# Kernel optimization log

Hardware: AMD Instinct MI355X
Metric: run time of the kernel (lower is better)

The kernel has to match this reference:

```python
import jax, jax.numpy as jnp
import numpy as np

LAMBDA_MAX = 2.0  # PyG ChebConv default when lambda_max is None and normalization='sym'
K = 3


def setup_inputs() -> dict:
    key = jax.random.key(0)
    ks = jax.random.split(key, 6)
    B, T, NT, Fin, Fout = 512, 24, 10, 256, 256
    N = B * NT
    E = 163840
    X = jax.random.normal(ks[0], (B, T, NT, Fin), dtype=jnp.float32)
    # edges without self loops (ChebConv removes them before building the Laplacian)
    rng = np.random.default_rng(0)
    src = rng.integers(0, N, size=E)
    off = rng.integers(1, N, size=E)
    dst = (src + off) % N
    edge_index = jnp.asarray(np.stack([src, dst]), dtype=jnp.int32)
    edge_weight = jax.random.uniform(ks[1], (E,), dtype=jnp.float32) + 0.1
    g = float(np.sqrt(6.0 / (Fin + Fout)))
    Ws = jax.random.uniform(ks[2], (4, Fin, Fout), minval=-g, maxval=g, dtype=jnp.float32)
    bs = jnp.zeros((4, Fout), jnp.float32)
    gc = float(np.sqrt(6.0 / (2 * Fout)))
    thetas = jax.random.uniform(ks[3], (4, K, Fout, Fout), minval=-gc, maxval=gc, dtype=jnp.float32)
    conv_bs = jnp.zeros((4, Fout), jnp.float32)
    return dict(X=X, edge_weight=edge_weight, Ws=Ws, bs=bs, thetas=thetas,
                conv_bs=conv_bs, edge_index=edge_index)


def _cheb_norm(edge_index, edge_weight, num_nodes):
    # L_hat = 2/lambda_max * (I - D^-1/2 A D^-1/2) - I
    src, dst = edge_index[0], edge_index[1]
    deg = jax.ops.segment_sum(edge_weight, src, num_segments=num_nodes)
    dis = jnp.where(deg > 0, jax.lax.rsqrt(jnp.where(deg > 0, deg, 1.0)), 0.0)
    w = -dis[src] * edge_weight * dis[dst]          # off-diagonal of L (sym)
    w_hat = (2.0 / LAMBDA_MAX) * w                  # scaled off-diagonal of L_hat
    diag = 2.0 / LAMBDA_MAX - 1.0                   # scalar diagonal of L_hat
    return w_hat, diag


def reference(X, edge_weight, Ws, bs, thetas, conv_bs, edge_index):
    B, T, NT, Fin = X.shape
    Fout = Ws.shape[-1]
    N = B * NT
    Xs = X.reshape(N, T, Fin).transpose(1, 0, 2)  # (T, N, Fin), matches torch .view
    src, dst = edge_index[0], edge_index[1]
    w_hat, diag = _cheb_norm(edge_index, edge_weight, N)

    def prop(x):  # L_hat @ x via edge scatter
        return jax.ops.segment_sum(w_hat[:, None] * x[src], dst, num_segments=N) + diag * x

    def cheb(x, theta, b):
        Tx0 = x
        out = Tx0 @ theta[0]
        Tx1 = prop(Tx0)
        out = out + Tx1 @ theta[1]
        for k in range(2, theta.shape[0]):
            Tx2 = 2.0 * prop(Tx1) - Tx0
            out = out + Tx2 @ theta[k]
            Tx0, Tx1 = Tx1, Tx2
        return out + b

    def step(carry, X_t):
        H, C = carry
        I = jax.nn.sigmoid(X_t @ Ws[0] + cheb(H, thetas[0], conv_bs[0]) + bs[0])
        Fg = jax.nn.sigmoid(X_t @ Ws[1] + cheb(H, thetas[1], conv_bs[1]) + bs[1])
        Tc = jnp.tanh(X_t @ Ws[2] + cheb(H, thetas[2], conv_bs[2]) + bs[2])
        C_new = Fg * C + I * Tc
        O = jax.nn.sigmoid(X_t @ Ws[3] + cheb(H, thetas[3], conv_bs[3]) + bs[3])
        H_new = O * jnp.tanh(C_new)
        return (H_new, C_new), None

    H0 = jnp.zeros((N, Fout), X.dtype)
    (H, C), _ = jax.lax.scan(step, (H0, H0), Xs)
    return H, C
```

## Files before the change

kernel.cpp:

```cpp
#include <hip/hip_runtime.h>
#include <cstddef>
#include <cstdint>

#define N_NODES 5120
#define E_EDGES 163840
#define F 256
#define TSTEPS 24
#define ND 1024
#define XROWSTRIDE 6144

typedef unsigned short u16;
typedef unsigned int u32;
typedef __bf16 bf16x8 __attribute__((ext_vector_type(8)));
typedef float f32x4 __attribute__((ext_vector_type(4)));

__device__ __forceinline__ u16 f2bf(float f) {
    u32 u = __float_as_uint(f);
    u = (u + 0x7FFFu + ((u >> 16) & 1u)) >> 16;
    return (u16)u;
}
__device__ __forceinline__ float bf2f(u16 h) {
    return __uint_as_float((u32)h << 16);
}
__device__ __forceinline__ float fsigmoid(float x) {
    return 1.f / (1.f + __expf(-x));
}
__device__ __forceinline__ float ftanh(float x) {
    return 1.f - 2.f / (__expf(2.f * x) + 1.f);
}


__global__ void deg_kernel(const float* __restrict__ ew, const int* __restrict__ src,
                           float* __restrict__ deg) {
    int e = blockIdx.x * 256 + threadIdx.x;
    if (e < E_EDGES) atomicAdd(&deg[src[e]], ew[e]);
}

__global__ void dis_kernel(float* __restrict__ deg) {
    int n = blockIdx.x * 256 + threadIdx.x;
    if (n < N_NODES) {
        float d = deg[n];
        deg[n] = d > 0.f ? rsqrtf(d) : 0.f;
    }
}

__global__ void count_kernel(const int* __restrict__ dst, int* __restrict__ cnt) {
    int e = blockIdx.x * 256 + threadIdx.x;
    if (e < E_EDGES) atomicAdd(&cnt[dst[e]], 1);
}

__global__ void scan_kernel(const int* __restrict__ cnt, int* __restrict__ row_ptr) {
    __shared__ int s[256];
    int tid = threadIdx.x;
    int base = tid * 20;
    int local[20];
    int sum = 0;
    #pragma unroll
    for (int i = 0; i < 20; i++) { local[i] = sum; sum += cnt[base + i]; }
    s[tid] = sum;
    __syncthreads();
    for (int off = 1; off < 256; off <<= 1) {
        int v = (tid >= off) ? s[tid - off] : 0;
        __syncthreads();
        s[tid] += v;
        __syncthreads();
    }
    int offset = (tid == 0) ? 0 : s[tid - 1];
    #pragma unroll
    for (int i = 0; i < 20; i++) row_ptr[base + i] = offset + local[i];
    if (tid == 0) row_ptr[N_NODES] = E_EDGES;
}

__global__ void fill_csr(const int* __restrict__ src, const int* __restrict__ dst,
                         const float* __restrict__ ew, const float* __restrict__ dis,
                         const int* __restrict__ row_ptr, int* __restrict__ cursor,
                         int* __restrict__ csr_src, float* __restrict__ csr_w) {
    int e = blockIdx.x * 256 + threadIdx.x;
    if (e >= E_EDGES) return;
    int s = src[e], d = dst[e];
    int pos = row_ptr[d] + atomicAdd(&cursor[d], 1);
    csr_src[pos] = s;
    csr_w[pos] = -dis[s] * ew[e] * dis[d];
}

__global__ void build_wcatT(const float* __restrict__ Ws, const float* __restrict__ thetas,
                            u16* __restrict__ WT) {
    int idx = blockIdx.x * 256 + threadIdx.x;
    if (idx >= 1024 * 1024) return;
    int c = idx >> 10, k = idx & 1023;
    int g = (c >> 4) & 3;
    int j = (c >> 6) * 16 + (c & 15);
    float v;
    if (k < 256) {
        v = Ws[(g * 256 + k) * 256 + j];
    } else {
        int kc = (k >> 8) - 1;
        int rr = k & 255;
        v = thetas[((g * 3 + kc) * 256 + rr) * 256 + j];
    }
    WT[idx] = f2bf(v);
}

__global__ void build_bsum(const float* __restrict__ bs, const float* __restrict__ cbs,
                           float* __restrict__ bsum) {
    int c = blockIdx.x * 256 + threadIdx.x;
    if (c >= 1024) return;
    int g = (c >> 4) & 3;
    int j = (c >> 6) * 16 + (c & 15);
    bsum[c] = bs[g * 256 + j] + cbs[g * 256 + j];
}


__global__ __launch_bounds__(256) void prop_kernel(
        const u16* __restrict__ xin, const u16* __restrict__ sub, float scale,
        const int* __restrict__ row_ptr, const int* __restrict__ csr_src,
        const float* __restrict__ csr_w, u16* __restrict__ out_bf,
        const float* __restrict__ X, int t, u16* __restrict__ xt_out) {
    __shared__ int s_src[4][64];
    __shared__ float s_w[4][64];
    int wid = threadIdx.x >> 6, l = threadIdx.x & 63;
    int n = blockIdx.x * 4 + wid;
    int start = row_ptr[n], end = row_ptr[n + 1];
    float acc0 = 0.f, acc1 = 0.f, acc2 = 0.f, acc3 = 0.f;
    int fb = l * 4;
    for (int base = start; base < end; base += 64) {
        int chunk = min(64, end - base);
        if (l < chunk) {
            s_src[wid][l] = csr_src[base + l];
            s_w[wid][l] = csr_w[base + l];
        }
        #pragma unroll 4
        for (int i = 0; i < chunk; i++) {
            int s = s_src[wid][i];
            float wt = s_w[wid][i];
            ushort4 hv = *(const ushort4*)(xin + (size_t)s * F + fb);
            acc0 += wt * bf2f(hv.x);
            acc1 += wt * bf2f(hv.y);
            acc2 += wt * bf2f(hv.z);
            acc3 += wt * bf2f(hv.w);
        }
    }
    size_t o = (size_t)n * F + fb;
    float r0 = scale * acc0, r1 = scale * acc1, r2 = scale * acc2, r3 = scale * acc3;
    if (sub) {
        ushort4 sv = *(const ushort4*)(sub + o);
        r0 -= bf2f(sv.x); r1 -= bf2f(sv.y); r2 -= bf2f(sv.z); r3 -= bf2f(sv.w);
    }
    ushort4 ov;
    ov.x = f2bf(r0); ov.y = f2bf(r1); ov.z = f2bf(r2); ov.w = f2bf(r3);
    *(ushort4*)(out_bf + o) = ov;
    if (xt_out) {
        float4 xv = *(const float4*)(X + (size_t)n * XROWSTRIDE + (size_t)t * F + fb);
        ushort4 xo;
        xo.x = f2bf(xv.x); xo.y = f2bf(xv.y); xo.z = f2bf(xv.z); xo.w = f2bf(xv.w);
        *(ushort4*)(xt_out + o) = xo;
    }
}

#define GBM 64
#define GBN 128
#define GBK 64

__global__ __launch_bounds__(256) void mfma_gemm(
        const u16* __restrict__ Xt, const u16* __restrict__ Hb,
        const u16* __restrict__ T1, const u16* __restrict__ T2,
        const u16* __restrict__ WT, const float* __restrict__ bsum,
        float* __restrict__ Cst, float* __restrict__ Hout, u16* __restrict__ HbNew,
        int writeH) {
    __shared__ alignas(16) u16 As[GBM * GBK];
    __shared__ alignas(16) u16 Bs[GBN * GBK];
    int tid = threadIdx.x;
    int w = tid >> 6, l = tid & 63;
    int m0 = blockIdx.x * GBM, n0 = blockIdx.y * GBN;
    int wm = (w >> 1) * 32, wn = (w & 1) * 64;

    int srow = l >> 3;
    int scol = 8 * ((l & 7) ^ srow);

    f32x4 acc[2][4] = {};

    for (int k0 = 0; k0 < 1024; k0 += GBK) {
        int seg = k0 >> 8;
        const u16* ab = (seg == 0) ? Xt : (seg == 1) ? Hb : (seg == 2) ? T1 : T2;
        ab += (k0 & 255);
        const u16* bb = WT + k0;
        #pragma unroll
        for (int i = 0; i < 2; i++) {
            int c = i * 4 + w;
            int row = c * 8 + srow;
            __builtin_amdgcn_global_load_lds(
                (const __attribute__((address_space(1))) u32*)(ab + (size_t)(m0 + row) * F + scol),
                (__attribute__((address_space(3))) u32*)(As + c * 512), 16, 0, 0);
        }
        #pragma unroll
        for (int i = 0; i < 4; i++) {
            int c = i * 4 + w;
            int row = c * 8 + srow;
            __builtin_amdgcn_global_load_lds(
                (const __attribute__((address_space(1))) u32*)(bb + (size_t)(n0 + row) * 1024 + scol),
                (__attribute__((address_space(3))) u32*)(Bs + c * 512), 16, 0, 0);
        }
        __syncthreads();
        #pragma unroll
        for (int kk = 0; kk < 2; kk++) {
            int kr = kk * 32 + (l >> 4) * 8;
            bf16x8 af[2], bfr[4];
            #pragma unroll
            for (int mf = 0; mf < 2; mf++) {
                int r = wm + mf * 16 + (l & 15);
                af[mf] = *(const bf16x8*)(As + r * GBK + (kr ^ ((r & 7) << 3)));
            }
            #pragma unroll
            for (int nf = 0; nf < 4; nf++) {
                int r = wn + nf * 16 + (l & 15);
                bfr[nf] = *(const bf16x8*)(Bs + r * GBK + (kr ^ ((r & 7) << 3)));
            }
            #pragma unroll
            for (int mf = 0; mf < 2; mf++)
                #pragma unroll
                for (int nf = 0; nf < 4; nf++)
                    acc[mf][nf] = __builtin_amdgcn_mfma_f32_16x16x32_bf16(
                        af[mf], bfr[nf], acc[mf][nf], 0, 0, 0);
        }
        __syncthreads();
    }

    int cr = (l >> 4) * 4, cc = l & 15;
    int feat = ((n0 >> 6) + (w & 1)) * 16 + cc;
    float bI = bsum[n0 + wn + 0  + cc];
    float bF = bsum[n0 + wn + 16 + cc];
    float bT = bsum[n0 + wn + 32 + cc];
    float bO = bsum[n0 + wn + 48 + cc];
    #pragma unroll
    for (int mf = 0; mf < 2; mf++) {
        #pragma unroll
        for (int r = 0; r < 4; r++) {
            int row = m0 + wm + mf * 16 + cr + r;
            size_t o = (size_t)row * F + feat;
            float I  = fsigmoid(acc[mf][0][r] + bI);
            float Fg = fsigmoid(acc[mf][1][r] + bF);
            float Tc = ftanh(acc[mf][2][r] + bT);
            float O  = fsigmoid(acc[mf][3][r] + bO);
            float c  = Fg * Cst[o] + I * Tc;
            Cst[o] = c;
            float h = O * ftanh(c);
            if (writeH) Hout[o] = h;
            HbNew[o] = f2bf(h);
        }
    }
}


extern "C" void kernel_launch(void* const* d_in, const int* in_sizes, int n_in,
                              void* d_out, int out_size, void* d_ws, size_t ws_size,
                              hipStream_t stream) {
    const float* X   = (const float*)d_in[0];
    const float* ew  = (const float*)d_in[1];
    const float* Ws  = (const float*)d_in[2];
    const float* bs  = (const float*)d_in[3];
    const float* th  = (const float*)d_in[4];
    const float* cbs = (const float*)d_in[5];
    const int*   ei  = (const int*)d_in[6];
    const int* src = ei;
    const int* dst = ei + E_EDGES;

    float* H = (float*)d_out;
    float* C = H + (size_t)N_NODES * F;

    char* w = (char*)d_ws;
    size_t off = 0;
    auto alloc = [&](size_t bytes) {
        void* p = w + off;
        off += (bytes + 255) & ~(size_t)255;
        return p;
    };
    float* deg     = (float*)alloc(N_NODES * 4);
    int*   cnt     = (int*)  alloc(N_NODES * 4);
    int*   cursor  = (int*)  alloc(N_NODES * 4);
    int*   row_ptr = (int*)  alloc((N_NODES + 1) * 4);
    int*   csr_src = (int*)  alloc(E_EDGES * 4);
    float* csr_w   = (float*)alloc(E_EDGES * 4);
    u16*   WT      = (u16*)  alloc((size_t)1024 * 1024 * 2);
    float* bsum    = (float*)alloc(1024 * 4);
    u16*   Xtbf    = (u16*)  alloc((size_t)N_NODES * F * 2);
    u16*   Hb0     = (u16*)  alloc((size_t)N_NODES * F * 2);
    u16*   Hb1     = (u16*)  alloc((size_t)N_NODES * F * 2);
    u16*   Tx1bf   = (u16*)  alloc((size_t)N_NODES * F * 2);
    u16*   Tx2bf   = (u16*)  alloc((size_t)N_NODES * F * 2);

    hipMemsetAsync(d_out, 0, (size_t)2 * N_NODES * F * 4, stream);
    hipMemsetAsync(Hb0, 0, (size_t)N_NODES * F * 2, stream);
    hipMemsetAsync(deg, 0, N_NODES * 4, stream);
    hipMemsetAsync(cnt, 0, N_NODES * 4, stream);
    hipMemsetAsync(cursor, 0, N_NODES * 4, stream);

    int eb = E_EDGES / 256;
    deg_kernel<<<eb, 256, 0, stream>>>(ew, src, deg);
    dis_kernel<<<N_NODES / 256, 256, 0, stream>>>(deg);
    count_kernel<<<eb, 256, 0, stream>>>(dst, cnt);
    scan_kernel<<<1, 256, 0, stream>>>(cnt, row_ptr);
    fill_csr<<<eb, 256, 0, stream>>>(src, dst, ew, deg, row_ptr, cursor, csr_src, csr_w);
    build_wcatT<<<(1024 * 1024) / 256, 256, 0, stream>>>(Ws, th, WT);
    build_bsum<<<4, 256, 0, stream>>>(bs, cbs, bsum);

    dim3 ggrid(N_NODES / GBM, ND / GBN);
    for (int t = 0; t < TSTEPS; t++) {
        u16* Hrd = (t & 1) ? Hb1 : Hb0;
        u16* Hwr = (t & 1) ? Hb0 : Hb1;
        prop_kernel<<<N_NODES / 4, 256, 0, stream>>>(Hrd, nullptr, 1.f, row_ptr, csr_src,
                                                     csr_w, Tx1bf, X, t, Xtbf);
        prop_kernel<<<N_NODES / 4, 256, 0, stream>>>(Tx1bf, Hrd, 2.f, row_ptr, csr_src,
                                                     csr_w, Tx2bf, nullptr, 0, nullptr);
        mfma_gemm<<<ggrid, 256, 0, stream>>>(Xtbf, Hrd, Tx1bf, Tx2bf, WT, bsum, C, H, Hwr,
                                             t == TSTEPS - 1 ? 1 : 0);
    }
}
```

Measured before the change: 1.010 ms.

## Load GEMM fragments directly from global memory, drop LDS staging and output memset

```diff
diff --git a/kernel.cpp b/kernel.cpp
--- a/kernel.cpp
+++ b/kernel.cpp
@@ -159,71 +159,53 @@
 
 #define GBM 64
 #define GBN 128
-#define GBK 64
-
-__global__ __launch_bounds__(256) void mfma_gemm(
+
+__global__ __launch_bounds__(256, 3) void mfma_gemm(
         const u16* __restrict__ Xt, const u16* __restrict__ Hb,
         const u16* __restrict__ T1, const u16* __restrict__ T2,
         const u16* __restrict__ WT, const float* __restrict__ bsum,
         float* __restrict__ Cst, float* __restrict__ Hout, u16* __restrict__ HbNew,
-        int writeH) {
-    __shared__ alignas(16) u16 As[GBM * GBK];
-    __shared__ alignas(16) u16 Bs[GBN * GBK];
+        int writeH, int isFirst) {
     int tid = threadIdx.x;
     int w = tid >> 6, l = tid & 63;
     int m0 = blockIdx.x * GBM, n0 = blockIdx.y * GBN;
     int wm = (w >> 1) * 32, wn = (w & 1) * 64;
-
-    int srow = l >> 3;
-    int scol = 8 * ((l & 7) ^ srow);
+    int rin = l & 15;
+    int kc = (l >> 4) * 8;
 
     f32x4 acc[2][4] = {};
 
-    for (int k0 = 0; k0 < 1024; k0 += GBK) {
-        int seg = k0 >> 8;
-        const u16* ab = (seg == 0) ? Xt : (seg == 1) ? Hb : (seg == 2) ? T1 : T2;
-        ab += (k0 & 255);
-        const u16* bb = WT + k0;
+    size_t a0 = (size_t)(m0 + wm + rin) * F + kc;
+    size_t a1 = a0 + (size_t)16 * F;
+    size_t b0 = (size_t)(n0 + wn + rin) * 1024 + kc;
+    size_t b1 = b0 + 16 * 1024;
+    size_t b2 = b0 + 32 * 1024;
+    size_t b3 = b0 + 48 * 1024;
+
+    auto seg = [&](const u16* __restrict__ ab, const u16* __restrict__ bb) {
         #pragma unroll
-        for (int i = 0; i < 2; i++) {
-            int c = i * 4 + w;
-            int row = c * 8 + srow;
-            __builtin_amdgcn_global_load_lds(
-                (const __attribute__((address_space(1))) u32*)(ab + (size_t)(m0 + row) * F + scol),
-                (__attribute__((address_space(3))) u32*)(As + c * 512), 16, 0, 0);
-        }
-        #pragma unroll
-        for (int i = 0; i < 4; i++) {
-            int c = i * 4 + w;
-            int row = c * 8 + srow;
-            __builtin_amdgcn_global_load_lds(
-                (const __attribute__((address_space(1))) u32*)(bb + (size_t)(n0 + row) * 1024 + scol),
-                (__attribute__((address_space(3))) u32*)(Bs + c * 512), 16, 0, 0);
-        }
-        __syncthreads();
-        #pragma unroll
-        for (int kk = 0; kk < 2; kk++) {
-            int kr = kk * 32 + (l >> 4) * 8;
-            bf16x8 af[2], bfr[4];
-            #pragma unroll
-            for (int mf = 0; mf < 2; mf++) {
-                int r = wm + mf * 16 + (l & 15);
-                af[mf] = *(const bf16x8*)(As + r * GBK + (kr ^ ((r & 7) << 3)));
-            }
-            #pragma unroll
-            for (int nf = 0; nf < 4; nf++) {
-                int r = wn + nf * 16 + (l & 15);
-                bfr[nf] = *(const bf16x8*)(Bs + r * GBK + (kr ^ ((r & 7) << 3)));
-            }
-            #pragma unroll
-            for (int mf = 0; mf < 2; mf++)
-                #pragma unroll
-                for (int nf = 0; nf < 4; nf++)
-                    acc[mf][nf] = __builtin_amdgcn_mfma_f32_16x16x32_bf16(
-                        af[mf], bfr[nf], acc[mf][nf], 0, 0, 0);
-        }
-        __syncthreads();
-    }
+        for (int kw = 0; kw < 8; kw++) {
+            int k = kw * 32;
+            bf16x8 av0 = *(const bf16x8*)(ab + a0 + k);
+            bf16x8 av1 = *(const bf16x8*)(ab + a1 + k);
+            bf16x8 bv0 = *(const bf16x8*)(bb + b0 + k);
+            bf16x8 bv1 = *(const bf16x8*)(bb + b1 + k);
+            bf16x8 bv2 = *(const bf16x8*)(bb + b2 + k);
+            bf16x8 bv3 = *(const bf16x8*)(bb + b3 + k);
+            acc[0][0] = __builtin_amdgcn_mfma_f32_16x16x32_bf16(av0, bv0, acc[0][0], 0, 0, 0);
+            acc[0][1] = __builtin_amdgcn_mfma_f32_16x16x32_bf16(av0, bv1, acc[0][1], 0, 0, 0);
+            acc[0][2] = __builtin_amdgcn_mfma_f32_16x16x32_bf16(av0, bv2, acc[0][2], 0, 0, 0);
+            acc[0][3] = __builtin_amdgcn_mfma_f32_16x16x32_bf16(av0, bv3, acc[0][3], 0, 0, 0);
+            acc[1][0] = __builtin_amdgcn_mfma_f32_16x16x32_bf16(av1, bv0, acc[1][0], 0, 0, 0);
+            acc[1][1] = __builtin_amdgcn_mfma_f32_16x16x32_bf16(av1, bv1, acc[1][1], 0, 0, 0);
+            acc[1][2] = __builtin_amdgcn_mfma_f32_16x16x32_bf16(av1, bv2, acc[1][2], 0, 0, 0);
+            acc[1][3] = __builtin_amdgcn_mfma_f32_16x16x32_bf16(av1, bv3, acc[1][3], 0, 0, 0);
+        }
+    };
+    seg(Xt, WT);
+    seg(Hb, WT + 256);
+    seg(T1, WT + 512);
+    seg(T2, WT + 768);
 
     int cr = (l >> 4) * 4, cc = l & 15;
     int feat = ((n0 >> 6) + (w & 1)) * 16 + cc;
@@ -241,7 +223,8 @@
             float Fg = fsigmoid(acc[mf][1][r] + bF);
             float Tc = ftanh(acc[mf][2][r] + bT);
             float O  = fsigmoid(acc[mf][3][r] + bO);
-            float c  = Fg * Cst[o] + I * Tc;
+            float cprev = isFirst ? 0.f : Cst[o];
+            float c  = Fg * cprev + I * Tc;
             Cst[o] = c;
             float h = O * ftanh(c);
             if (writeH) Hout[o] = h;
@@ -288,7 +271,6 @@
     u16*   Tx1bf   = (u16*)  alloc((size_t)N_NODES * F * 2);
     u16*   Tx2bf   = (u16*)  alloc((size_t)N_NODES * F * 2);
 
-    hipMemsetAsync(d_out, 0, (size_t)2 * N_NODES * F * 4, stream);
     hipMemsetAsync(Hb0, 0, (size_t)N_NODES * F * 2, stream);
     hipMemsetAsync(deg, 0, N_NODES * 4, stream);
     hipMemsetAsync(cnt, 0, N_NODES * 4, stream);
@@ -312,6 +294,6 @@
         prop_kernel<<<N_NODES / 4, 256, 0, stream>>>(Tx1bf, Hrd, 2.f, row_ptr, csr_src,
                                                      csr_w, Tx2bf, nullptr, 0, nullptr);
         mfma_gemm<<<ggrid, 256, 0, stream>>>(Xtbf, Hrd, Tx1bf, Tx2bf, WT, bsum, C, H, Hwr,
-                                             t == TSTEPS - 1 ? 1 : 0);
-    }
-}
+                                             t == TSTEPS - 1 ? 1 : 0, t == 0 ? 1 : 0);
+    }
+}
```

New measurement: 2.176 ms. 2.15x slower.

## Retile gate GEMM to 80-row blocks with 8-wide gate interleave and lane shuffles

Applied to the files above, without the earlier changes.

```diff
diff --git a/kernel.cpp b/kernel.cpp
--- a/kernel.cpp
+++ b/kernel.cpp
@@ -88,8 +88,8 @@
     int idx = blockIdx.x * 256 + threadIdx.x;
     if (idx >= 1024 * 1024) return;
     int c = idx >> 10, k = idx & 1023;
-    int g = (c >> 4) & 3;
-    int j = (c >> 6) * 16 + (c & 15);
+    int g = (c >> 3) & 3;
+    int j = (c >> 5) * 8 + (c & 7);
     float v;
     if (k < 256) {
         v = Ws[(g * 256 + k) * 256 + j];
@@ -105,8 +105,8 @@
                            float* __restrict__ bsum) {
     int c = blockIdx.x * 256 + threadIdx.x;
     if (c >= 1024) return;
-    int g = (c >> 4) & 3;
-    int j = (c >> 6) * 16 + (c & 15);
+    int g = (c >> 3) & 3;
+    int j = (c >> 5) * 8 + (c & 7);
     bsum[c] = bs[g * 256 + j] + cbs[g * 256 + j];
 }
 
@@ -157,7 +157,7 @@
     }
 }
 
-#define GBM 64
+#define GBM 80
 #define GBN 128
 #define GBK 64
 
@@ -166,27 +166,29 @@
         const u16* __restrict__ T1, const u16* __restrict__ T2,
         const u16* __restrict__ WT, const float* __restrict__ bsum,
         float* __restrict__ Cst, float* __restrict__ Hout, u16* __restrict__ HbNew,
-        int writeH) {
+        int writeH, int isFirst) {
     __shared__ alignas(16) u16 As[GBM * GBK];
     __shared__ alignas(16) u16 Bs[GBN * GBK];
     int tid = threadIdx.x;
     int w = tid >> 6, l = tid & 63;
     int m0 = blockIdx.x * GBM, n0 = blockIdx.y * GBN;
-    int wm = (w >> 1) * 32, wn = (w & 1) * 64;
+    int wn = w * 32;
 
     int srow = l >> 3;
     int scol = 8 * ((l & 7) ^ srow);
 
-    f32x4 acc[2][4] = {};
+    int nA = (w < 2) ? 3 : 2;
+    int cA0 = (w < 2) ? w * 3 : 6 + (w - 2) * 2;
+
+    f32x4 acc[5][2] = {};
 
     for (int k0 = 0; k0 < 1024; k0 += GBK) {
         int seg = k0 >> 8;
         const u16* ab = (seg == 0) ? Xt : (seg == 1) ? Hb : (seg == 2) ? T1 : T2;
         ab += (k0 & 255);
         const u16* bb = WT + k0;
-        #pragma unroll
-        for (int i = 0; i < 2; i++) {
-            int c = i * 4 + w;
+        for (int i = 0; i < nA; i++) {
+            int c = cA0 + i;
             int row = c * 8 + srow;
             __builtin_amdgcn_global_load_lds(
                 (const __attribute__((address_space(1))) u32*)(ab + (size_t)(m0 + row) * F + scol),
@@ -204,21 +206,21 @@
         #pragma unroll
         for (int kk = 0; kk < 2; kk++) {
             int kr = kk * 32 + (l >> 4) * 8;
-            bf16x8 af[2], bfr[4];
+            bf16x8 af[5], bfr[2];
             #pragma unroll
-            for (int mf = 0; mf < 2; mf++) {
-                int r = wm + mf * 16 + (l & 15);
+            for (int mf = 0; mf < 5; mf++) {
+                int r = mf * 16 + (l & 15);
                 af[mf] = *(const bf16x8*)(As + r * GBK + (kr ^ ((r & 7) << 3)));
             }
             #pragma unroll
-            for (int nf = 0; nf < 4; nf++) {
+            for (int nf = 0; nf < 2; nf++) {
                 int r = wn + nf * 16 + (l & 15);
                 bfr[nf] = *(const bf16x8*)(Bs + r * GBK + (kr ^ ((r & 7) << 3)));
             }
             #pragma unroll
-            for (int mf = 0; mf < 2; mf++)
+            for (int mf = 0; mf < 5; mf++)
                 #pragma unroll
-                for (int nf = 0; nf < 4; nf++)
+                for (int nf = 0; nf < 2; nf++)
                     acc[mf][nf] = __builtin_amdgcn_mfma_f32_16x16x32_bf16(
                         af[mf], bfr[nf], acc[mf][nf], 0, 0, 0);
         }
@@ -226,22 +228,38 @@
     }
 
     int cr = (l >> 4) * 4, cc = l & 15;
-    int feat = ((n0 >> 6) + (w & 1)) * 16 + cc;
-    float bI = bsum[n0 + wn + 0  + cc];
-    float bF = bsum[n0 + wn + 16 + cc];
-    float bT = bsum[n0 + wn + 32 + cc];
-    float bO = bsum[n0 + wn + 48 + cc];
+    int half = cc >> 3, f8 = cc & 7;
+    int nb = n0 + wn;
+    int feat = (nb >> 5) * 8 + f8;
+    float bI = bsum[nb + f8];
+    float bF = bsum[nb + 8 + f8];
+    float bT = bsum[nb + 16 + f8];
+    float bO = bsum[nb + 24 + f8];
     #pragma unroll
-    for (int mf = 0; mf < 2; mf++) {
+    for (int mf = 0; mf < 5; mf++) {
+        float own0[4], own1[4], rec0[4], rec1[4];
         #pragma unroll
-        for (int r = 0; r < 4; r++) {
-            int row = m0 + wm + mf * 16 + cr + r;
+        for (int rg = 0; rg < 4; rg++) {
+            own0[rg] = acc[mf][0][rg];
+            own1[rg] = acc[mf][1][rg];
+            rec0[rg] = __shfl_xor(own0[rg], 8, 64);
+            rec1[rg] = __shfl_xor(own1[rg], 8, 64);
+        }
+        #pragma unroll
+        for (int q = 0; q < 2; q++) {
+            int rg = half * 2 + q;
+            float vI = half ? rec0[rg] : own0[rg];
+            float vF = half ? own0[rg] : rec0[rg];
+            float vT = half ? rec1[rg] : own1[rg];
+            float vO = half ? own1[rg] : rec1[rg];
+            int row = m0 + mf * 16 + cr + rg;
             size_t o = (size_t)row * F + feat;
-            float I  = fsigmoid(acc[mf][0][r] + bI);
-            float Fg = fsigmoid(acc[mf][1][r] + bF);
-            float Tc = ftanh(acc[mf][2][r] + bT);
-            float O  = fsigmoid(acc[mf][3][r] + bO);
-            float c  = Fg * Cst[o] + I * Tc;
+            float I  = fsigmoid(vI + bI);
+            float Fg = fsigmoid(vF + bF);
+            float Tc = ftanh(vT + bT);
+            float O  = fsigmoid(vO + bO);
+            float cprev = isFirst ? 0.f : Cst[o];
+            float c  = Fg * cprev + I * Tc;
             Cst[o] = c;
             float h = O * ftanh(c);
             if (writeH) Hout[o] = h;
@@ -288,7 +306,6 @@
     u16*   Tx1bf   = (u16*)  alloc((size_t)N_NODES * F * 2);
     u16*   Tx2bf   = (u16*)  alloc((size_t)N_NODES * F * 2);
 
-    hipMemsetAsync(d_out, 0, (size_t)2 * N_NODES * F * 4, stream);
     hipMemsetAsync(Hb0, 0, (size_t)N_NODES * F * 2, stream);
     hipMemsetAsync(deg, 0, N_NODES * 4, stream);
     hipMemsetAsync(cnt, 0, N_NODES * 4, stream);
@@ -312,6 +329,6 @@
         prop_kernel<<<N_NODES / 4, 256, 0, stream>>>(Tx1bf, Hrd, 2.f, row_ptr, csr_src,
                                                      csr_w, Tx2bf, nullptr, 0, nullptr);
         mfma_gemm<<<ggrid, 256, 0, stream>>>(Xtbf, Hrd, Tx1bf, Tx2bf, WT, bsum, C, H, Hwr,
-                                             t == TSTEPS - 1 ? 1 : 0);
-    }
-}
+                                             t == TSTEPS - 1 ? 1 : 0, t == 0 ? 1 : 0);
+    }
+}
```

Result: slower. 1.188 ms (+17.7%).

## Precompute input projection X@W for all timesteps in one batched GEMM

Applied to the files above, without the earlier changes.

```diff
diff --git a/kernel.cpp b/kernel.cpp
--- a/kernel.cpp
+++ b/kernel.cpp
@@ -8,6 +8,7 @@
 #define TSTEPS 24
 #define ND 1024
 #define XROWSTRIDE 6144
+#define MROWS (N_NODES * TSTEPS)
 
 typedef unsigned short u16;
 typedef unsigned int u32;
@@ -110,12 +111,97 @@
     bsum[c] = bs[g * 256 + j] + cbs[g * 256 + j];
 }
 
+__global__ void conv_x(const float* __restrict__ X, u16* __restrict__ Xbf) {
+    size_t i = (size_t)blockIdx.x * 256 + threadIdx.x;
+    float4 v = ((const float4*)X)[i];
+    ushort4 o;
+    o.x = f2bf(v.x); o.y = f2bf(v.y); o.z = f2bf(v.z); o.w = f2bf(v.w);
+    ((ushort4*)Xbf)[i] = o;
+}
+
+#define GBM 64
+#define GBN 128
+#define GBK 64
+
+__global__ __launch_bounds__(256) void xw_gemm(
+        const u16* __restrict__ Xbf, const u16* __restrict__ WT,
+        u16* __restrict__ XW) {
+    __shared__ alignas(16) u16 As[GBM * GBK];
+    __shared__ alignas(16) u16 Bs[GBN * GBK];
+    int tid = threadIdx.x;
+    int w = tid >> 6, l = tid & 63;
+    int m0 = blockIdx.x * GBM, n0 = blockIdx.y * GBN;
+    int wm = (w >> 1) * 32, wn = (w & 1) * 64;
+    int srow = l >> 3;
+    int scol = 8 * ((l & 7) ^ srow);
+
+    f32x4 acc[2][4] = {};
+
+    for (int k0 = 0; k0 < 256; k0 += GBK) {
+        const u16* ab = Xbf + k0;
+        const u16* bb = WT + k0;
+        #pragma unroll
+        for (int i = 0; i < 2; i++) {
+            int c = i * 4 + w;
+            int row = c * 8 + srow;
+            __builtin_amdgcn_global_load_lds(
+                (const __attribute__((address_space(1))) u32*)(ab + (size_t)(m0 + row) * F + scol),
+                (__attribute__((address_space(3))) u32*)(As + c * 512), 16, 0, 0);
+        }
+        #pragma unroll
+        for (int i = 0; i < 4; i++) {
+            int c = i * 4 + w;
+            int row = c * 8 + srow;
+            __builtin_amdgcn_global_load_lds(
+                (const __attribute__((address_space(1))) u32*)(bb + (size_t)(n0 + row) * 1024 + scol),
+                (__attribute__((address_space(3))) u32*)(Bs + c * 512), 16, 0, 0);
+        }
+        __syncthreads();
+        #pragma unroll
+        for (int kk = 0; kk < 2; kk++) {
+            int kr = kk * 32 + (l >> 4) * 8;
+            bf16x8 af[2], bfr[4];
+            #pragma unroll
+            for (int mf = 0; mf < 2; mf++) {
+                int r = wm + mf * 16 + (l & 15);
+                af[mf] = *(const bf16x8*)(As + r * GBK + (kr ^ ((r & 7) << 3)));
+            }
+            #pragma unroll
+            for (int nf = 0; nf < 4; nf++) {
+                int r = wn + nf * 16 + (l & 15);
+                bfr[nf] = *(const bf16x8*)(Bs + r * GBK + (kr ^ ((r & 7) << 3)));
+            }
+            #pragma unroll
+            for (int mf = 0; mf < 2; mf++)
+                #pragma unroll
+                for (int nf = 0; nf < 4; nf++)
+                    acc[mf][nf] = __builtin_amdgcn_mfma_f32_16x16x32_bf16(
+                        af[mf], bfr[nf], acc[mf][nf], 0, 0, 0);
+        }
+        __syncthreads();
+    }
+
+    int cr = (l >> 4) * 4, cc = l & 15;
+    #pragma unroll
+    for (int mf = 0; mf < 2; mf++) {
+        #pragma unroll
+        for (int rg = 0; rg < 4; rg++) {
+            int r = m0 + wm + mf * 16 + cr + rg;
+            int n = r / 24;
+            int t = r - n * 24;
+            size_t base = (size_t)t * N_NODES * ND + (size_t)n * ND + n0 + wn + cc;
+            #pragma unroll
+            for (int nf = 0; nf < 4; nf++)
+                XW[base + nf * 16] = f2bf(acc[mf][nf][rg]);
+        }
+    }
+}
+
 
 __global__ __launch_bounds__(256) void prop_kernel(
         const u16* __restrict__ xin, const u16* __restrict__ sub, float scale,
         const int* __restrict__ row_ptr, const int* __restrict__ csr_src,
-        const float* __restrict__ csr_w, u16* __restrict__ out_bf,
-        const float* __restrict__ X, int t, u16* __restrict__ xt_out) {
+        const float* __restrict__ csr_w, u16* __restrict__ out_bf) {
     __shared__ int s_src[4][64];
     __shared__ float s_w[4][64];
     int wid = threadIdx.x >> 6, l = threadIdx.x & 63;
@@ -149,41 +235,32 @@
     ushort4 ov;
     ov.x = f2bf(r0); ov.y = f2bf(r1); ov.z = f2bf(r2); ov.w = f2bf(r3);
     *(ushort4*)(out_bf + o) = ov;
-    if (xt_out) {
-        float4 xv = *(const float4*)(X + (size_t)n * XROWSTRIDE + (size_t)t * F + fb);
-        ushort4 xo;
-        xo.x = f2bf(xv.x); xo.y = f2bf(xv.y); xo.z = f2bf(xv.z); xo.w = f2bf(xv.w);
-        *(ushort4*)(xt_out + o) = xo;
-    }
-}
-
-#define GBM 64
-#define GBN 128
-#define GBK 64
+}
+
+#define NKS 12
 
 __global__ __launch_bounds__(256) void mfma_gemm(
-        const u16* __restrict__ Xt, const u16* __restrict__ Hb,
-        const u16* __restrict__ T1, const u16* __restrict__ T2,
-        const u16* __restrict__ WT, const float* __restrict__ bsum,
+        const u16* __restrict__ Hb, const u16* __restrict__ T1,
+        const u16* __restrict__ T2, const u16* __restrict__ WT,
+        const u16* __restrict__ XWt, const float* __restrict__ bsum,
         float* __restrict__ Cst, float* __restrict__ Hout, u16* __restrict__ HbNew,
-        int writeH) {
+        int writeH, int isFirst) {
     __shared__ alignas(16) u16 As[GBM * GBK];
     __shared__ alignas(16) u16 Bs[GBN * GBK];
     int tid = threadIdx.x;
     int w = tid >> 6, l = tid & 63;
     int m0 = blockIdx.x * GBM, n0 = blockIdx.y * GBN;
     int wm = (w >> 1) * 32, wn = (w & 1) * 64;
-
     int srow = l >> 3;
     int scol = 8 * ((l & 7) ^ srow);
 
     f32x4 acc[2][4] = {};
 
-    for (int k0 = 0; k0 < 1024; k0 += GBK) {
+    for (int k0 = 0; k0 < 768; k0 += GBK) {
         int seg = k0 >> 8;
-        const u16* ab = (seg == 0) ? Xt : (seg == 1) ? Hb : (seg == 2) ? T1 : T2;
+        const u16* ab = (seg == 0) ? Hb : (seg == 1) ? T1 : T2;
         ab += (k0 & 255);
-        const u16* bb = WT + k0;
+        const u16* bb = WT + 256 + k0;
         #pragma unroll
         for (int i = 0; i < 2; i++) {
             int c = i * 4 + w;
@@ -236,12 +313,18 @@
         #pragma unroll
         for (int r = 0; r < 4; r++) {
             int row = m0 + wm + mf * 16 + cr + r;
+            size_t xb = (size_t)row * ND + n0 + wn + cc;
+            float xI = bf2f(XWt[xb + 0]);
+            float xF = bf2f(XWt[xb + 16]);
+            float xT = bf2f(XWt[xb + 32]);
+            float xO = bf2f(XWt[xb + 48]);
             size_t o = (size_t)row * F + feat;
-            float I  = fsigmoid(acc[mf][0][r] + bI);
-            float Fg = fsigmoid(acc[mf][1][r] + bF);
-            float Tc = ftanh(acc[mf][2][r] + bT);
-            float O  = fsigmoid(acc[mf][3][r] + bO);
-            float c  = Fg * Cst[o] + I * Tc;
+            float I  = fsigmoid(acc[mf][0][r] + xI + bI);
+            float Fg = fsigmoid(acc[mf][1][r] + xF + bF);
+            float Tc = ftanh(acc[mf][2][r] + xT + bT);
+            float O  = fsigmoid(acc[mf][3][r] + xO + bO);
+            float cprev = isFirst ? 0.f : Cst[o];
+            float c  = Fg * cprev + I * Tc;
             Cst[o] = c;
             float h = O * ftanh(c);
             if (writeH) Hout[o] = h;
@@ -282,13 +365,13 @@
     float* csr_w   = (float*)alloc(E_EDGES * 4);
     u16*   WT      = (u16*)  alloc((size_t)1024 * 1024 * 2);
     float* bsum    = (float*)alloc(1024 * 4);
-    u16*   Xtbf    = (u16*)  alloc((size_t)N_NODES * F * 2);
     u16*   Hb0     = (u16*)  alloc((size_t)N_NODES * F * 2);
     u16*   Hb1     = (u16*)  alloc((size_t)N_NODES * F * 2);
     u16*   Tx1bf   = (u16*)  alloc((size_t)N_NODES * F * 2);
     u16*   Tx2bf   = (u16*)  alloc((size_t)N_NODES * F * 2);
-
-    hipMemsetAsync(d_out, 0, (size_t)2 * N_NODES * F * 4, stream);
+    u16*   Xbf     = (u16*)  alloc((size_t)MROWS * F * 2);
+    u16*   XW      = (u16*)  alloc((size_t)TSTEPS * N_NODES * ND * 2);
+
     hipMemsetAsync(Hb0, 0, (size_t)N_NODES * F * 2, stream);
     hipMemsetAsync(deg, 0, N_NODES * 4, stream);
     hipMemsetAsync(cnt, 0, N_NODES * 4, stream);
@@ -303,15 +386,21 @@
     build_wcatT<<<(1024 * 1024) / 256, 256, 0, stream>>>(Ws, th, WT);
     build_bsum<<<4, 256, 0, stream>>>(bs, cbs, bsum);
 
+    conv_x<<<(MROWS * F / 4) / 256, 256, 0, stream>>>(X, Xbf);
+    dim3 xwgrid(MROWS / GBM, ND / GBN);
+    xw_gemm<<<xwgrid, 256, 0, stream>>>(Xbf, WT, XW);
+
     dim3 ggrid(N_NODES / GBM, ND / GBN);
     for (int t = 0; t < TSTEPS; t++) {
         u16* Hrd = (t & 1) ? Hb1 : Hb0;
         u16* Hwr = (t & 1) ? Hb0 : Hb1;
         prop_kernel<<<N_NODES / 4, 256, 0, stream>>>(Hrd, nullptr, 1.f, row_ptr, csr_src,
-                                                     csr_w, Tx1bf, X, t, Xtbf);
+                                                     csr_w, Tx1bf);
         prop_kernel<<<N_NODES / 4, 256, 0, stream>>>(Tx1bf, Hrd, 2.f, row_ptr, csr_src,
-                                                     csr_w, Tx2bf, nullptr, 0, nullptr);
-        mfma_gemm<<<ggrid, 256, 0, stream>>>(Xtbf, Hrd, Tx1bf, Tx2bf, WT, bsum, C, H, Hwr,
-                                             t == TSTEPS - 1 ? 1 : 0);
-    }
-}
+                                                     csr_w, Tx2bf);
+        mfma_gemm<<<ggrid, 256, 0, stream>>>(Hrd, Tx1bf, Tx2bf, WT,
+                                             XW + (size_t)t * N_NODES * ND, bsum,
+                                             C, H, Hwr,
+                                             t == TSTEPS - 1 ? 1 : 0, t == 0 ? 1 : 0);
+    }
+}
```

Measured after the change: 1.121 ms. +11.0%, slower.
